# Kernel optimization log

Measured on AMD Instinct MI355X. Metric: run time of the kernel, lower is better.

The kernel has to match this reference:

```python
import jax, jax.numpy as jnp
import numpy as np

N, E, D, L, G = 10000, 320000, 256, 5, 128
RWSE, DEG_V = 16, 1001
BN_EPS = 1e-5


def setup_inputs() -> dict:
    key = jax.random.key(0)
    ks = jax.random.split(key, 12)
    s = 1.0 / np.sqrt(D)
    return {
        'feat_id': jax.random.randint(ks[0], (N,), 0, 100000, dtype=jnp.int64 if jax.config.jax_enable_x64 else jnp.int32),
        'edge_index': jax.random.randint(ks[1], (2, E), 0, N),
        'batch_idx': jnp.sort(jax.random.randint(ks[2], (N,), 0, G)),
        'rwse': jax.random.normal(ks[3], (N, RWSE), jnp.float32),
        'in_degrees': jax.random.randint(ks[4], (N,), 0, DEG_V),
        # value_projection: Linear(fixed_input_dim=D -> D); stored as [in, out]
        'w_val': jax.random.normal(ks[5], (D, D), jnp.float32) * s,
        'b_val': jnp.zeros((D,), jnp.float32),
        # rwse_projection: Linear(RWSE -> D)
        'w_rwse': jax.random.normal(ks[6], (RWSE, D), jnp.float32) * (1.0 / np.sqrt(RWSE)),
        'b_rwse': jnp.zeros((D,), jnp.float32),
        # degree_embedding table (clamped to [0, 1000])
        'deg_emb': jax.random.normal(ks[7], (DEG_V, D), jnp.float32) * 0.02,
        # per-layer GIN MLP: Linear-ReLU-Linear, stacked over L layers
        'mlp_w1': jax.random.normal(ks[8], (L, D, D), jnp.float32) * s,
        'mlp_b1': jnp.zeros((L, D), jnp.float32),
        'mlp_w2': jax.random.normal(ks[9], (L, D, D), jnp.float32) * s,
        'mlp_b2': jnp.zeros((L, D), jnp.float32),
        # BatchNorm1d (eval mode: running stats)
        'bn_gamma': jnp.ones((L, D), jnp.float32),
        'bn_beta': jnp.zeros((L, D), jnp.float32),
        'bn_mean': jnp.zeros((L, D), jnp.float32),
        'bn_var': jax.random.uniform(ks[10], (L, D), jnp.float32, 0.5, 1.5),
        # GIN eps per layer
        'eps_gin': jnp.zeros((L,), jnp.float32),
    }


def reference(feat_id, edge_index, batch_idx, rwse, in_degrees,
              w_val, b_val, w_rwse, b_rwse, deg_emb,
              mlp_w1, mlp_b1, mlp_w2, mlp_b2,
              bn_gamma, bn_beta, bn_mean, bn_var, eps_gin):
    # --- node feature embedding ---
    h_id = jnp.remainder(feat_id, D)
    h_one = jax.nn.one_hot(h_id, D, dtype=jnp.float32)            # [N, D]
    h = h_one @ w_val + b_val + rwse @ w_rwse + b_rwse            # value + rwse projections
    deg = jnp.clip(in_degrees, 0, 1000)
    h = h + deg_emb[deg]                                          # degree embedding

    src, dst = edge_index[0], edge_index[1]
    for l in range(L):
        # GIN message passing: sum neighbor features into dst (gather -> scatter-add)
        agg = jax.ops.segment_sum(h[src], dst, num_segments=N)    # [N, D]
        y = agg + (1.0 + eps_gin[l]) * h
        # MLP (Linear-ReLU-Linear)
        y = jax.nn.relu(y @ mlp_w1[l] + mlp_b1[l]) @ mlp_w2[l] + mlp_b2[l]
        # BatchNorm1d (eval: running stats) + ReLU
        y = (y - bn_mean[l]) * (bn_gamma[l] * jax.lax.rsqrt(bn_var[l] + BN_EPS)) + bn_beta[l]
        h = jax.nn.relu(y)

    # --- mean pooling per graph ---
    sums = jax.ops.segment_sum(h, batch_idx, num_segments=G)                     # [G, D]
    cnt = jax.ops.segment_sum(jnp.ones((N, 1), h.dtype), batch_idx, num_segments=G)
    graph_feature = sums / jnp.maximum(cnt, 1.0)
    return graph_feature, h
```

## Files before the change

### kernel.cpp

```cpp
#include <hip/hip_runtime.h>
#include <hip/hip_bf16.h>

#define N_NODES 10000
#define N_EDGES 320000
#define DIM     256
#define N_LAYERS 5
#define N_GRAPHS 128
#define RWSE_K  16

typedef __bf16 bf16_t;
typedef bf16_t bf16x8 __attribute__((ext_vector_type(8)));
typedef float  f32x4  __attribute__((ext_vector_type(4)));

__device__ inline ushort f2bf(float f) {
    union { float f; unsigned u; } v; v.f = f;
    unsigned r = v.u + 0x7fff + ((v.u >> 16) & 1);
    return (ushort)(r >> 16);
}
__device__ inline float bfbits2f(unsigned hi16) {
    union { unsigned u; float f; } v; v.u = hi16;
    return v.f;
}

__global__ __launch_bounds__(256)
void setup_kernel(const int* __restrict__ feat_id,
                  const float* __restrict__ rwse,
                  const int* __restrict__ in_deg,
                  const float* __restrict__ w_val,
                  const float* __restrict__ b_val,
                  const float* __restrict__ w_rwse,
                  const float* __restrict__ b_rwse,
                  const float* __restrict__ deg_emb,
                  float* __restrict__ h, ushort* __restrict__ hb,
                  const int* __restrict__ ei, int* __restrict__ cnt_arr,
                  const float* __restrict__ w1, const float* __restrict__ w2,
                  ushort* __restrict__ wt1, ushort* __restrict__ wt2,
                  const float* __restrict__ gamma, const float* __restrict__ beta,
                  const float* __restrict__ mean, const float* __restrict__ var,
                  const float* __restrict__ b2, float* __restrict__ scale,
                  float* __restrict__ shift) {
    __shared__ float r[RWSE_K];
    __shared__ float t[32][33];
    int b = blockIdx.x;
    int tid = threadIdx.x;
    if (b < N_NODES) {
        int i = b, d = tid;
        if (d < RWSE_K) r[d] = rwse[i * RWSE_K + d];
        __syncthreads();
        int hid = feat_id[i] & (DIM - 1);
        int dg = in_deg[i];
        dg = dg < 0 ? 0 : (dg > 1000 ? 1000 : dg);
        float v = w_val[hid * DIM + d] + b_val[d] + b_rwse[d] + deg_emb[dg * DIM + d];
#pragma unroll
        for (int k = 0; k < RWSE_K; ++k) v += r[k] * w_rwse[k * DIM + d];
        h[i * DIM + d] = v;
        hb[i * DIM + d] = f2bf(v);
    } else if (b < 11250) {
        int e = (b - N_NODES) * 256 + tid;
        if (e < N_EDGES) atomicAdd(&cnt_arr[ei[N_EDGES + e]], 1);
    } else if (b < 11890) {
        int w_id = b - 11250;
        int l = w_id >> 7;
        int rem = w_id & 127;
        int mat = rem >> 6;
        int tile = rem & 63;
        const float* W  = (mat ? w2  : w1)  + (size_t)l * DIM * DIM;
        ushort*      Wt = (mat ? wt2 : wt1) + (size_t)l * DIM * DIM;
        int k0 = (tile >> 3) * 32, n0 = (tile & 7) * 32;
        int tx = tid & 31, ty = tid >> 5;
#pragma unroll
        for (int j = 0; j < 4; ++j)
            t[ty + j * 8][tx] = W[(k0 + ty + j * 8) * DIM + n0 + tx];
        __syncthreads();
#pragma unroll
        for (int j = 0; j < 4; ++j)
            Wt[(n0 + ty + j * 8) * DIM + k0 + tx] = f2bf(t[tx][ty + j * 8]);
    } else {
        int l = b - 11890;
        int idx = l * DIM + tid;
        float s = gamma[idx] * rsqrtf(var[idx] + 1e-5f);
        scale[idx] = s;
        shift[idx] = beta[idx] + (b2[idx] - mean[idx]) * s;
    }
}

__global__ __launch_bounds__(1024)
void scan_kernel(const int* __restrict__ cnt_arr, int* __restrict__ cur, int n) {
    __shared__ int wsum[16];
    __shared__ int carry_sh;
    int tid = threadIdx.x, wave = tid >> 6, lane = tid & 63;
    if (tid == 0) carry_sh = 0;
    __syncthreads();
    for (int base = 0; base < n; base += 1024) {
        int idx = base + tid;
        int v = (idx < n) ? cnt_arr[idx] : 0;
        int s = v;
#pragma unroll
        for (int off = 1; off < 64; off <<= 1) {
            int t = __shfl_up(s, off, 64);
            if (lane >= off) s += t;
        }
        if (lane == 63) wsum[wave] = s;
        __syncthreads();
        if (wave == 0) {
            int ws = (lane < 16) ? wsum[lane] : 0;
#pragma unroll
            for (int off = 1; off < 16; off <<= 1) {
                int t = __shfl_up(ws, off, 64);
                if (lane >= off) ws += t;
            }
            if (lane < 16) wsum[lane] = ws;
        }
        __syncthreads();
        int excl = s - v + (wave ? wsum[wave - 1] : 0) + carry_sh;
        if (idx < n) cur[idx] = excl;
        __syncthreads();
        if (tid == 0) carry_sh += wsum[15];
        __syncthreads();
    }
}

__global__ __launch_bounds__(256)
void fill_kernel(const int* __restrict__ ei, int* __restrict__ cur,
                 int* __restrict__ cs) {
    int e = blockIdx.x * 256 + threadIdx.x;
    if (e < N_EDGES) {
        int d = ei[N_EDGES + e];
        int p = atomicAdd(&cur[d], 1);
        cs[p] = ei[e];
    }
}

__global__ __launch_bounds__(256)
void agg_kernel(const float* __restrict__ h, const ushort* __restrict__ hb,
                const int* __restrict__ cur, const int* __restrict__ cs,
                const float* __restrict__ eps_gin, int layer,
                ushort* __restrict__ y) {
    int wave = threadIdx.x >> 6;
    int lane = threadIdx.x & 63;
    int half = lane >> 5;
    int sl   = lane & 31;
    int i = blockIdx.x * 4 + wave;
    if (i >= N_NODES) return;
    const uint4* hb4 = (const uint4*)hb;
    float acc[8];
#pragma unroll
    for (int t = 0; t < 8; ++t) acc[t] = 0.f;

    int e0 = i ? cur[i - 1] : 0;
    int e1 = cur[i];
    for (int base = e0; base < e1; base += 64) {
        int rem = e1 - base;
        int cnt = rem < 64 ? rem : 64;
        int idx = (base + lane < e1) ? cs[base + lane] : 0;
        int j = 0;
        for (; j + 8 <= cnt; j += 8) {
            int s0 = __shfl(idx, j + half, 64);
            int s1 = __shfl(idx, j + 2 + half, 64);
            int s2 = __shfl(idx, j + 4 + half, 64);
            int s3 = __shfl(idx, j + 6 + half, 64);
            uint4 v0 = hb4[(size_t)s0 * 32 + sl];
            uint4 v1 = hb4[(size_t)s1 * 32 + sl];
            uint4 v2 = hb4[(size_t)s2 * 32 + sl];
            uint4 v3 = hb4[(size_t)s3 * 32 + sl];
            acc[0] += bfbits2f(v0.x << 16); acc[1] += bfbits2f(v0.x & 0xffff0000u);
            acc[2] += bfbits2f(v0.y << 16); acc[3] += bfbits2f(v0.y & 0xffff0000u);
            acc[4] += bfbits2f(v0.z << 16); acc[5] += bfbits2f(v0.z & 0xffff0000u);
            acc[6] += bfbits2f(v0.w << 16); acc[7] += bfbits2f(v0.w & 0xffff0000u);
            acc[0] += bfbits2f(v1.x << 16); acc[1] += bfbits2f(v1.x & 0xffff0000u);
            acc[2] += bfbits2f(v1.y << 16); acc[3] += bfbits2f(v1.y & 0xffff0000u);
            acc[4] += bfbits2f(v1.z << 16); acc[5] += bfbits2f(v1.z & 0xffff0000u);
            acc[6] += bfbits2f(v1.w << 16); acc[7] += bfbits2f(v1.w & 0xffff0000u);
            acc[0] += bfbits2f(v2.x << 16); acc[1] += bfbits2f(v2.x & 0xffff0000u);
            acc[2] += bfbits2f(v2.y << 16); acc[3] += bfbits2f(v2.y & 0xffff0000u);
            acc[4] += bfbits2f(v2.z << 16); acc[5] += bfbits2f(v2.z & 0xffff0000u);
            acc[6] += bfbits2f(v2.w << 16); acc[7] += bfbits2f(v2.w & 0xffff0000u);
            acc[0] += bfbits2f(v3.x << 16); acc[1] += bfbits2f(v3.x & 0xffff0000u);
            acc[2] += bfbits2f(v3.y << 16); acc[3] += bfbits2f(v3.y & 0xffff0000u);
            acc[4] += bfbits2f(v3.z << 16); acc[5] += bfbits2f(v3.z & 0xffff0000u);
            acc[6] += bfbits2f(v3.w << 16); acc[7] += bfbits2f(v3.w & 0xffff0000u);
        }
        for (; j + 2 <= cnt; j += 2) {
            int s = __shfl(idx, j + half, 64);
            uint4 v = hb4[(size_t)s * 32 + sl];
            acc[0] += bfbits2f(v.x << 16); acc[1] += bfbits2f(v.x & 0xffff0000u);
            acc[2] += bfbits2f(v.y << 16); acc[3] += bfbits2f(v.y & 0xffff0000u);
            acc[4] += bfbits2f(v.z << 16); acc[5] += bfbits2f(v.z & 0xffff0000u);
            acc[6] += bfbits2f(v.w << 16); acc[7] += bfbits2f(v.w & 0xffff0000u);
        }
        if (j < cnt) {
            int s = __shfl(idx, j, 64);
            if (half == 0) {
                uint4 v = hb4[(size_t)s * 32 + sl];
                acc[0] += bfbits2f(v.x << 16); acc[1] += bfbits2f(v.x & 0xffff0000u);
                acc[2] += bfbits2f(v.y << 16); acc[3] += bfbits2f(v.y & 0xffff0000u);
                acc[4] += bfbits2f(v.z << 16); acc[5] += bfbits2f(v.z & 0xffff0000u);
                acc[6] += bfbits2f(v.w << 16); acc[7] += bfbits2f(v.w & 0xffff0000u);
            }
        }
    }
#pragma unroll
    for (int t = 0; t < 8; ++t) acc[t] += __shfl_xor(acc[t], 32, 64);
    if (half == 0) {
        float sc = 1.0f + eps_gin[layer];
        const float4* h4 = (const float4*)h;
        float4 a0 = h4[(size_t)i * 64 + sl * 2];
        float4 a1 = h4[(size_t)i * 64 + sl * 2 + 1];
        acc[0] += a0.x * sc; acc[1] += a0.y * sc;
        acc[2] += a0.z * sc; acc[3] += a0.w * sc;
        acc[4] += a1.x * sc; acc[5] += a1.y * sc;
        acc[6] += a1.z * sc; acc[7] += a1.w * sc;
        uint4 o;
        o.x = (uint)f2bf(acc[0]) | ((uint)f2bf(acc[1]) << 16);
        o.y = (uint)f2bf(acc[2]) | ((uint)f2bf(acc[3]) << 16);
        o.z = (uint)f2bf(acc[4]) | ((uint)f2bf(acc[5]) << 16);
        o.w = (uint)f2bf(acc[6]) | ((uint)f2bf(acc[7]) << 16);
        ((uint4*)y)[(size_t)i * 32 + sl] = o;
    }
}

#define GBM 32

__global__ __launch_bounds__(256)
void gemm12_kernel(const ushort* __restrict__ A, const ushort* __restrict__ Wt1,
                   const float* __restrict__ b1, const ushort* __restrict__ Wt2,
                   const float* __restrict__ bnsc, const float* __restrict__ bnsh,
                   float* __restrict__ H, ushort* __restrict__ Hb, int nrows) {
    __shared__ __align__(16) ushort As[GBM][40];
    __shared__ __align__(16) ushort Bs[DIM][40];
    __shared__ __align__(16) ushort Ts[GBM][DIM + 8];
    int tx = threadIdx.x;
    int row0 = blockIdx.x * GBM;
    int wave = tx >> 6, lane = tx & 63, quad = lane >> 4, l16 = lane & 15;
    int wr = (wave >> 1) * 16;
    int wc = (wave & 1) * 128;
    int srow = tx >> 2;
    int skol = (tx & 3) * 8;

    f32x4 acc[8];
#pragma unroll
    for (int t = 0; t < 8; ++t) acc[t] = (f32x4){0.f, 0.f, 0.f, 0.f};

    for (int k0 = 0; k0 < DIM; k0 += 32) {
        if (tx < 128) {
            int arow = row0 + srow;
            uint4 av = make_uint4(0u, 0u, 0u, 0u);
            if (arow < nrows) av = *(const uint4*)&A[(size_t)arow * DIM + k0 + skol];
            *(uint4*)&As[srow][skol] = av;
        }
#pragma unroll
        for (int j = 0; j < 4; ++j) {
            int r = srow + 64 * j;
            *(uint4*)&Bs[r][skol] = *(const uint4*)&Wt1[(size_t)r * DIM + k0 + skol];
        }
        __syncthreads();
        bf16x8 af = *(const bf16x8*)&As[wr + l16][quad * 8];
#pragma unroll
        for (int tj = 0; tj < 8; ++tj) {
            bf16x8 bf = *(const bf16x8*)&Bs[wc + tj * 16 + l16][quad * 8];
            acc[tj] = __builtin_amdgcn_mfma_f32_16x16x32_bf16(af, bf, acc[tj], 0, 0, 0);
        }
        __syncthreads();
    }
#pragma unroll
    for (int tj = 0; tj < 8; ++tj) {
        int col = wc + tj * 16 + l16;
        float bias = b1[col];
#pragma unroll
        for (int r = 0; r < 4; ++r) {
            int rl = wr + quad * 4 + r;
            Ts[rl][col] = f2bf(fmaxf(acc[tj][r] + bias, 0.f));
        }
    }
    __syncthreads();

#pragma unroll
    for (int t = 0; t < 8; ++t) acc[t] = (f32x4){0.f, 0.f, 0.f, 0.f};
    for (int k0 = 0; k0 < DIM; k0 += 32) {
#pragma unroll
        for (int j = 0; j < 4; ++j) {
            int r = srow + 64 * j;
            *(uint4*)&Bs[r][skol] = *(const uint4*)&Wt2[(size_t)r * DIM + k0 + skol];
        }
        __syncthreads();
        bf16x8 af = *(const bf16x8*)&Ts[wr + l16][k0 + quad * 8];
#pragma unroll
        for (int tj = 0; tj < 8; ++tj) {
            bf16x8 bf = *(const bf16x8*)&Bs[wc + tj * 16 + l16][quad * 8];
            acc[tj] = __builtin_amdgcn_mfma_f32_16x16x32_bf16(af, bf, acc[tj], 0, 0, 0);
        }
        __syncthreads();
    }
#pragma unroll
    for (int tj = 0; tj < 8; ++tj) {
        int col = wc + tj * 16 + l16;
        float s = bnsc[col], sh = bnsh[col];
#pragma unroll
        for (int r = 0; r < 4; ++r) {
            int row = row0 + wr + quad * 4 + r;
            if (row < nrows) {
                float v = fmaxf(acc[tj][r] * s + sh, 0.f);
                H[(size_t)row * DIM + col] = v;
                Hb[(size_t)row * DIM + col] = f2bf(v);
            }
        }
    }
}

__global__ __launch_bounds__(256)
void pool_kernel(const float* __restrict__ hfin, const int* __restrict__ batch,
                 float* __restrict__ out) {
    int g = blockIdx.x;
    int d = threadIdx.x;
    int l = 0, r = N_NODES;
    while (l < r) { int m = (l + r) >> 1; if (batch[m] < g) l = m + 1; else r = m; }
    int lo = l;
    r = N_NODES;
    while (l < r) { int m = (l + r) >> 1; if (batch[m] < g + 1) l = m + 1; else r = m; }
    int hi = l;
    float a0 = 0.f, a1 = 0.f, a2 = 0.f, a3 = 0.f;
    int i = lo;
    for (; i + 4 <= hi; i += 4) {
        a0 += hfin[(size_t)i * DIM + d];
        a1 += hfin[(size_t)(i + 1) * DIM + d];
        a2 += hfin[(size_t)(i + 2) * DIM + d];
        a3 += hfin[(size_t)(i + 3) * DIM + d];
    }
    for (; i < hi; ++i) a0 += hfin[(size_t)i * DIM + d];
    float c = (float)(hi - lo);
    if (c < 1.f) c = 1.f;
    out[g * DIM + d] = ((a0 + a1) + (a2 + a3)) / c;
}

extern "C" void kernel_launch(void* const* d_in, const int* in_sizes, int n_in,
                              void* d_out, int out_size, void* d_ws, size_t ws_size,
                              hipStream_t stream) {
    const int*   feat_id  = (const int*)d_in[0];
    const int*   ei       = (const int*)d_in[1];
    const int*   batch    = (const int*)d_in[2];
    const float* rwse     = (const float*)d_in[3];
    const int*   in_deg   = (const int*)d_in[4];
    const float* w_val    = (const float*)d_in[5];
    const float* b_val    = (const float*)d_in[6];
    const float* w_rwse   = (const float*)d_in[7];
    const float* b_rwse   = (const float*)d_in[8];
    const float* deg_emb  = (const float*)d_in[9];
    const float* mlp_w1   = (const float*)d_in[10];
    const float* mlp_b1   = (const float*)d_in[11];
    const float* mlp_w2   = (const float*)d_in[12];
    const float* mlp_b2   = (const float*)d_in[13];
    const float* bn_gamma = (const float*)d_in[14];
    const float* bn_beta  = (const float*)d_in[15];
    const float* bn_mean  = (const float*)d_in[16];
    const float* bn_var   = (const float*)d_in[17];
    const float* eps_gin  = (const float*)d_in[18];

    float* out = (float*)d_out;
    float* out_h = out + N_GRAPHS * DIM;

    char* w = (char*)d_ws;
    float*  h   = (float*)w;
    ushort* hb  = (ushort*)(h + (size_t)N_NODES * DIM);
    ushort* y   = hb + (size_t)N_NODES * DIM;
    ushort* wt1 = y + (size_t)N_NODES * DIM;
    ushort* wt2 = wt1 + (size_t)N_LAYERS * DIM * DIM;
    int* cnt_arr = (int*)(wt2 + (size_t)N_LAYERS * DIM * DIM);
    int* cur     = cnt_arr + N_NODES;
    int* cs      = cur + N_NODES;
    float* bnsc  = (float*)(cs + N_EDGES);
    float* bnsh  = bnsc + N_LAYERS * DIM;

    hipMemsetAsync(cnt_arr, 0, N_NODES * sizeof(int), stream);

    setup_kernel<<<11895, 256, 0, stream>>>(
        feat_id, rwse, in_deg, w_val, b_val, w_rwse, b_rwse, deg_emb, h, hb,
        ei, cnt_arr, mlp_w1, mlp_w2, wt1, wt2,
        bn_gamma, bn_beta, bn_mean, bn_var, mlp_b2, bnsc, bnsh);
    scan_kernel<<<1, 1024, 0, stream>>>(cnt_arr, cur, N_NODES);
    fill_kernel<<<(N_EDGES + 255) / 256, 256, 0, stream>>>(ei, cur, cs);

    int ggrid = (N_NODES + GBM - 1) / GBM;
    for (int l = 0; l < N_LAYERS; ++l) {
        agg_kernel<<<(N_NODES + 3) / 4, 256, 0, stream>>>(h, hb, cur, cs, eps_gin, l, y);
        float* Hdst = (l == N_LAYERS - 1) ? out_h : h;
        gemm12_kernel<<<ggrid, 256, 0, stream>>>(y, wt1 + (size_t)l * DIM * DIM,
                                                 mlp_b1 + l * DIM,
                                                 wt2 + (size_t)l * DIM * DIM,
                                                 bnsc + l * DIM, bnsh + l * DIM,
                                                 Hdst, hb, N_NODES);
    }

    pool_kernel<<<N_GRAPHS, 256, 0, stream>>>(out_h, batch, out);
}
```

Measured before the change: 362.7 us.

## Replace LDS-staged MLP GEMM with single-wave register-tiled kernel; scalarize agg index loads

The fused two-GEMM MLP kernel is rewritten so that one 64-thread wave owns a 32-row tile. It reads A and weight fragments straight from global memory instead of staging them through shared memory, and keeps 32 accumulators in registers, which removes the block-wide __syncthreads barriers. The aggregation kernel makes the edge range wave-uniform and loads neighbor indices directly instead of shuffling them, and the bf16 copy of h is no longer written on the last layer. The trade-offs are heavy register pressure, low occupancy from 64-thread blocks, and weight reads that now depend on L1/L2 hits rather than LDS reuse.

Result: slower. 610.0 us (+68.2%).

```diff
diff --git a/kernel.cpp b/kernel.cpp
--- a/kernel.cpp
+++ b/kernel.cpp
@@ -131,6 +131,12 @@
     }
 }
 
+#define ACCV(v)                                                        \
+    acc[0] += bfbits2f((v).x << 16); acc[1] += bfbits2f((v).x & 0xffff0000u); \
+    acc[2] += bfbits2f((v).y << 16); acc[3] += bfbits2f((v).y & 0xffff0000u); \
+    acc[4] += bfbits2f((v).z << 16); acc[5] += bfbits2f((v).z & 0xffff0000u); \
+    acc[6] += bfbits2f((v).w << 16); acc[7] += bfbits2f((v).w & 0xffff0000u);
+
 __global__ __launch_bounds__(256)
 void agg_kernel(const float* __restrict__ h, const ushort* __restrict__ hb,
                 const int* __restrict__ cur, const int* __restrict__ cs,
@@ -149,54 +155,34 @@
 
     int e0 = i ? cur[i - 1] : 0;
     int e1 = cur[i];
-    for (int base = e0; base < e1; base += 64) {
-        int rem = e1 - base;
-        int cnt = rem < 64 ? rem : 64;
-        int idx = (base + lane < e1) ? cs[base + lane] : 0;
-        int j = 0;
-        for (; j + 8 <= cnt; j += 8) {
-            int s0 = __shfl(idx, j + half, 64);
-            int s1 = __shfl(idx, j + 2 + half, 64);
-            int s2 = __shfl(idx, j + 4 + half, 64);
-            int s3 = __shfl(idx, j + 6 + half, 64);
-            uint4 v0 = hb4[(size_t)s0 * 32 + sl];
-            uint4 v1 = hb4[(size_t)s1 * 32 + sl];
-            uint4 v2 = hb4[(size_t)s2 * 32 + sl];
-            uint4 v3 = hb4[(size_t)s3 * 32 + sl];
-            acc[0] += bfbits2f(v0.x << 16); acc[1] += bfbits2f(v0.x & 0xffff0000u);
-            acc[2] += bfbits2f(v0.y << 16); acc[3] += bfbits2f(v0.y & 0xffff0000u);
-            acc[4] += bfbits2f(v0.z << 16); acc[5] += bfbits2f(v0.z & 0xffff0000u);
-            acc[6] += bfbits2f(v0.w << 16); acc[7] += bfbits2f(v0.w & 0xffff0000u);
-            acc[0] += bfbits2f(v1.x << 16); acc[1] += bfbits2f(v1.x & 0xffff0000u);
-            acc[2] += bfbits2f(v1.y << 16); acc[3] += bfbits2f(v1.y & 0xffff0000u);
-            acc[4] += bfbits2f(v1.z << 16); acc[5] += bfbits2f(v1.z & 0xffff0000u);
-            acc[6] += bfbits2f(v1.w << 16); acc[7] += bfbits2f(v1.w & 0xffff0000u);
-            acc[0] += bfbits2f(v2.x << 16); acc[1] += bfbits2f(v2.x & 0xffff0000u);
-            acc[2] += bfbits2f(v2.y << 16); acc[3] += bfbits2f(v2.y & 0xffff0000u);
-            acc[4] += bfbits2f(v2.z << 16); acc[5] += bfbits2f(v2.z & 0xffff0000u);
-            acc[6] += bfbits2f(v2.w << 16); acc[7] += bfbits2f(v2.w & 0xffff0000u);
-            acc[0] += bfbits2f(v3.x << 16); acc[1] += bfbits2f(v3.x & 0xffff0000u);
-            acc[2] += bfbits2f(v3.y << 16); acc[3] += bfbits2f(v3.y & 0xffff0000u);
-            acc[4] += bfbits2f(v3.z << 16); acc[5] += bfbits2f(v3.z & 0xffff0000u);
-            acc[6] += bfbits2f(v3.w << 16); acc[7] += bfbits2f(v3.w & 0xffff0000u);
-        }
-        for (; j + 2 <= cnt; j += 2) {
-            int s = __shfl(idx, j + half, 64);
-            uint4 v = hb4[(size_t)s * 32 + sl];
-            acc[0] += bfbits2f(v.x << 16); acc[1] += bfbits2f(v.x & 0xffff0000u);
-            acc[2] += bfbits2f(v.y << 16); acc[3] += bfbits2f(v.y & 0xffff0000u);
-            acc[4] += bfbits2f(v.z << 16); acc[5] += bfbits2f(v.z & 0xffff0000u);
-            acc[6] += bfbits2f(v.w << 16); acc[7] += bfbits2f(v.w & 0xffff0000u);
-        }
-        if (j < cnt) {
-            int s = __shfl(idx, j, 64);
-            if (half == 0) {
-                uint4 v = hb4[(size_t)s * 32 + sl];
-                acc[0] += bfbits2f(v.x << 16); acc[1] += bfbits2f(v.x & 0xffff0000u);
-                acc[2] += bfbits2f(v.y << 16); acc[3] += bfbits2f(v.y & 0xffff0000u);
-                acc[4] += bfbits2f(v.z << 16); acc[5] += bfbits2f(v.z & 0xffff0000u);
-                acc[6] += bfbits2f(v.w << 16); acc[7] += bfbits2f(v.w & 0xffff0000u);
-            }
+    e0 = __builtin_amdgcn_readfirstlane(e0);
+    e1 = __builtin_amdgcn_readfirstlane(e1);
+
+    int e = e0;
+    for (; e + 8 <= e1; e += 8) {
+        int n0 = cs[e + 0], n1 = cs[e + 1], n2 = cs[e + 2], n3 = cs[e + 3];
+        int n4 = cs[e + 4], n5 = cs[e + 5], n6 = cs[e + 6], n7 = cs[e + 7];
+        int s0 = half ? n1 : n0;
+        int s1 = half ? n3 : n2;
+        int s2 = half ? n5 : n4;
+        int s3 = half ? n7 : n6;
+        uint4 v0 = hb4[(size_t)s0 * 32 + sl];
+        uint4 v1 = hb4[(size_t)s1 * 32 + sl];
+        uint4 v2 = hb4[(size_t)s2 * 32 + sl];
+        uint4 v3 = hb4[(size_t)s3 * 32 + sl];
+        ACCV(v0); ACCV(v1); ACCV(v2); ACCV(v3);
+    }
+    for (; e + 2 <= e1; e += 2) {
+        int n0 = cs[e], n1 = cs[e + 1];
+        int s = half ? n1 : n0;
+        uint4 v = hb4[(size_t)s * 32 + sl];
+        ACCV(v);
+    }
+    if (e < e1) {
+        int n0 = cs[e];
+        if (!half) {
+            uint4 v = hb4[(size_t)n0 * 32 + sl];
+            ACCV(v);
         }
     }
 #pragma unroll
@@ -219,91 +205,81 @@
     }
 }
 
-#define GBM 32
-
-__global__ __launch_bounds__(256)
-void gemm12_kernel(const ushort* __restrict__ A, const ushort* __restrict__ Wt1,
-                   const float* __restrict__ b1, const ushort* __restrict__ Wt2,
-                   const float* __restrict__ bnsc, const float* __restrict__ bnsh,
-                   float* __restrict__ H, ushort* __restrict__ Hb, int nrows) {
-    __shared__ __align__(16) ushort As[GBM][40];
-    __shared__ __align__(16) ushort Bs[DIM][40];
-    __shared__ __align__(16) ushort Ts[GBM][DIM + 8];
-    int tx = threadIdx.x;
-    int row0 = blockIdx.x * GBM;
-    int wave = tx >> 6, lane = tx & 63, quad = lane >> 4, l16 = lane & 15;
-    int wr = (wave >> 1) * 16;
-    int wc = (wave & 1) * 128;
-    int srow = tx >> 2;
-    int skol = (tx & 3) * 8;
-
-    f32x4 acc[8];
-#pragma unroll
-    for (int t = 0; t < 8; ++t) acc[t] = (f32x4){0.f, 0.f, 0.f, 0.f};
+#define MROWS 32
+#define MTILES ((N_NODES + MROWS - 1) / MROWS)
+
+__global__ __launch_bounds__(64)
+void mlp_kernel(const ushort* __restrict__ A, const ushort* __restrict__ Wt1,
+                const float* __restrict__ b1, const ushort* __restrict__ Wt2,
+                const float* __restrict__ bnsc, const float* __restrict__ bnsh,
+                float* __restrict__ H, ushort* __restrict__ Hb, int nrows) {
+    __shared__ __align__(16) ushort t_lds[MROWS][DIM + 8];
+    int lane = threadIdx.x;
+    int quad = lane >> 4, l16 = lane & 15;
+    int row0 = blockIdx.x * MROWS;
+    int r0 = row0 + l16;
+    int r1 = row0 + 16 + l16;
+
+    f32x4 acc[2][16];
+#pragma unroll
+    for (int mg = 0; mg < 2; ++mg)
+#pragma unroll
+        for (int tj = 0; tj < 16; ++tj) acc[mg][tj] = (f32x4){0.f, 0.f, 0.f, 0.f};
+
+    const bf16x8 zf = (bf16x8){0, 0, 0, 0, 0, 0, 0, 0};
 
     for (int k0 = 0; k0 < DIM; k0 += 32) {
-        if (tx < 128) {
-            int arow = row0 + srow;
-            uint4 av = make_uint4(0u, 0u, 0u, 0u);
-            if (arow < nrows) av = *(const uint4*)&A[(size_t)arow * DIM + k0 + skol];
-            *(uint4*)&As[srow][skol] = av;
-        }
-#pragma unroll
-        for (int j = 0; j < 4; ++j) {
-            int r = srow + 64 * j;
-            *(uint4*)&Bs[r][skol] = *(const uint4*)&Wt1[(size_t)r * DIM + k0 + skol];
-        }
-        __syncthreads();
-        bf16x8 af = *(const bf16x8*)&As[wr + l16][quad * 8];
-#pragma unroll
-        for (int tj = 0; tj < 8; ++tj) {
-            bf16x8 bf = *(const bf16x8*)&Bs[wc + tj * 16 + l16][quad * 8];
-            acc[tj] = __builtin_amdgcn_mfma_f32_16x16x32_bf16(af, bf, acc[tj], 0, 0, 0);
-        }
-        __syncthreads();
-    }
-#pragma unroll
-    for (int tj = 0; tj < 8; ++tj) {
-        int col = wc + tj * 16 + l16;
+        int ko = k0 + quad * 8;
+        bf16x8 a0 = (r0 < nrows) ? *(const bf16x8*)&A[(size_t)r0 * DIM + ko] : zf;
+        bf16x8 a1 = (r1 < nrows) ? *(const bf16x8*)&A[(size_t)r1 * DIM + ko] : zf;
+#pragma unroll
+        for (int tj = 0; tj < 16; ++tj) {
+            bf16x8 bfr = *(const bf16x8*)&Wt1[(size_t)(tj * 16 + l16) * DIM + ko];
+            acc[0][tj] = __builtin_amdgcn_mfma_f32_16x16x32_bf16(a0, bfr, acc[0][tj], 0, 0, 0);
+            acc[1][tj] = __builtin_amdgcn_mfma_f32_16x16x32_bf16(a1, bfr, acc[1][tj], 0, 0, 0);
+        }
+    }
+#pragma unroll
+    for (int tj = 0; tj < 16; ++tj) {
+        int col = tj * 16 + l16;
         float bias = b1[col];
 #pragma unroll
-        for (int r = 0; r < 4; ++r) {
-            int rl = wr + quad * 4 + r;
-            Ts[rl][col] = f2bf(fmaxf(acc[tj][r] + bias, 0.f));
-        }
-    }
-    __syncthreads();
-
-#pragma unroll
-    for (int t = 0; t < 8; ++t) acc[t] = (f32x4){0.f, 0.f, 0.f, 0.f};
+        for (int mg = 0; mg < 2; ++mg)
+#pragma unroll
+            for (int r = 0; r < 4; ++r)
+                t_lds[mg * 16 + quad * 4 + r][col] = f2bf(fmaxf(acc[mg][tj][r] + bias, 0.f));
+    }
+
+#pragma unroll
+    for (int mg = 0; mg < 2; ++mg)
+#pragma unroll
+        for (int tj = 0; tj < 16; ++tj) acc[mg][tj] = (f32x4){0.f, 0.f, 0.f, 0.f};
     for (int k0 = 0; k0 < DIM; k0 += 32) {
-#pragma unroll
-        for (int j = 0; j < 4; ++j) {
-            int r = srow + 64 * j;
-            *(uint4*)&Bs[r][skol] = *(const uint4*)&Wt2[(size_t)r * DIM + k0 + skol];
-        }
-        __syncthreads();
-        bf16x8 af = *(const bf16x8*)&Ts[wr + l16][k0 + quad * 8];
-#pragma unroll
-        for (int tj = 0; tj < 8; ++tj) {
-            bf16x8 bf = *(const bf16x8*)&Bs[wc + tj * 16 + l16][quad * 8];
-            acc[tj] = __builtin_amdgcn_mfma_f32_16x16x32_bf16(af, bf, acc[tj], 0, 0, 0);
-        }
-        __syncthreads();
-    }
-#pragma unroll
-    for (int tj = 0; tj < 8; ++tj) {
-        int col = wc + tj * 16 + l16;
+        int ko = k0 + quad * 8;
+        bf16x8 a0 = *(const bf16x8*)&t_lds[l16][ko];
+        bf16x8 a1 = *(const bf16x8*)&t_lds[16 + l16][ko];
+#pragma unroll
+        for (int tj = 0; tj < 16; ++tj) {
+            bf16x8 bfr = *(const bf16x8*)&Wt2[(size_t)(tj * 16 + l16) * DIM + ko];
+            acc[0][tj] = __builtin_amdgcn_mfma_f32_16x16x32_bf16(a0, bfr, acc[0][tj], 0, 0, 0);
+            acc[1][tj] = __builtin_amdgcn_mfma_f32_16x16x32_bf16(a1, bfr, acc[1][tj], 0, 0, 0);
+        }
+    }
+#pragma unroll
+    for (int tj = 0; tj < 16; ++tj) {
+        int col = tj * 16 + l16;
         float s = bnsc[col], sh = bnsh[col];
 #pragma unroll
-        for (int r = 0; r < 4; ++r) {
-            int row = row0 + wr + quad * 4 + r;
-            if (row < nrows) {
-                float v = fmaxf(acc[tj][r] * s + sh, 0.f);
-                H[(size_t)row * DIM + col] = v;
-                Hb[(size_t)row * DIM + col] = f2bf(v);
+        for (int mg = 0; mg < 2; ++mg)
+#pragma unroll
+            for (int r = 0; r < 4; ++r) {
+                int row = row0 + mg * 16 + quad * 4 + r;
+                if (row < nrows) {
+                    float v = fmaxf(acc[mg][tj][r] * s + sh, 0.f);
+                    H[(size_t)row * DIM + col] = v;
+                    if (Hb) Hb[(size_t)row * DIM + col] = f2bf(v);
+                }
             }
-        }
     }
 }
 
@@ -379,15 +355,15 @@
     scan_kernel<<<1, 1024, 0, stream>>>(cnt_arr, cur, N_NODES);
     fill_kernel<<<(N_EDGES + 255) / 256, 256, 0, stream>>>(ei, cur, cs);
 
-    int ggrid = (N_NODES + GBM - 1) / GBM;
     for (int l = 0; l < N_LAYERS; ++l) {
         agg_kernel<<<(N_NODES + 3) / 4, 256, 0, stream>>>(h, hb, cur, cs, eps_gin, l, y);
         float* Hdst = (l == N_LAYERS - 1) ? out_h : h;
-        gemm12_kernel<<<ggrid, 256, 0, stream>>>(y, wt1 + (size_t)l * DIM * DIM,
-                                                 mlp_b1 + l * DIM,
-                                                 wt2 + (size_t)l * DIM * DIM,
-                                                 bnsc + l * DIM, bnsh + l * DIM,
-                                                 Hdst, hb, N_NODES);
+        ushort* Hbdst = (l == N_LAYERS - 1) ? nullptr : hb;
+        mlp_kernel<<<MTILES, 64, 0, stream>>>(y, wt1 + (size_t)l * DIM * DIM,
+                                              mlp_b1 + l * DIM,
+                                              wt2 + (size_t)l * DIM * DIM,
+                                              bnsc + l * DIM, bnsh + l * DIM,
+                                              Hdst, Hbdst, N_NODES);
     }
 
     pool_kernel<<<N_GRAPHS, 256, 0, stream>>>(out_h, batch, out);
```

## Split bf16 node features into column halves and aggregate each half separately

Applied to the files above, without the earlier changes.

Node features are stored as two separate bf16 arrays, one per 128-column half, and the gather-aggregate kernel runs twice per layer, once per half. Each gathered table is half the size, so it is more likely to stay in cache during the random neighbor gather. The fp32 copy of h is dropped: the self term now reads the bf16 copy, and the GEMM writes fp32 output only on the last layer. The cost is an extra kernel launch per layer, repeated CSR index reads, and slightly lower precision in the self term.

After: 382.1 us. +5.4%, slower.

```diff
diff --git a/kernel.cpp b/kernel.cpp
--- a/kernel.cpp
+++ b/kernel.cpp
@@ -4,6 +4,7 @@
 #define N_NODES 10000
 #define N_EDGES 320000
 #define DIM     256
+#define HDIM    128
 #define N_LAYERS 5
 #define N_GRAPHS 128
 #define RWSE_K  16
@@ -31,7 +32,7 @@
                   const float* __restrict__ w_rwse,
                   const float* __restrict__ b_rwse,
                   const float* __restrict__ deg_emb,
-                  float* __restrict__ h, ushort* __restrict__ hb,
+                  ushort* __restrict__ hb_lo, ushort* __restrict__ hb_hi,
                   const int* __restrict__ ei, int* __restrict__ cnt_arr,
                   const float* __restrict__ w1, const float* __restrict__ w2,
                   ushort* __restrict__ wt1, ushort* __restrict__ wt2,
@@ -53,8 +54,8 @@
         float v = w_val[hid * DIM + d] + b_val[d] + b_rwse[d] + deg_emb[dg * DIM + d];
 #pragma unroll
         for (int k = 0; k < RWSE_K; ++k) v += r[k] * w_rwse[k * DIM + d];
-        h[i * DIM + d] = v;
-        hb[i * DIM + d] = f2bf(v);
+        int hh = d >> 7, dl = d & (HDIM - 1);
+        (hh ? hb_hi : hb_lo)[i * HDIM + dl] = f2bf(v);
     } else if (b < 11250) {
         int e = (b - N_NODES) * 256 + tid;
         if (e < N_EDGES) atomicAdd(&cnt_arr[ei[N_EDGES + e]], 1);
@@ -131,18 +132,24 @@
     }
 }
 
-__global__ __launch_bounds__(256)
-void agg_kernel(const float* __restrict__ h, const ushort* __restrict__ hb,
+#define ACCV(v)                                                        \
+    acc[0] += bfbits2f((v).x << 16); acc[1] += bfbits2f((v).x & 0xffff0000u); \
+    acc[2] += bfbits2f((v).y << 16); acc[3] += bfbits2f((v).y & 0xffff0000u); \
+    acc[4] += bfbits2f((v).z << 16); acc[5] += bfbits2f((v).z & 0xffff0000u); \
+    acc[6] += bfbits2f((v).w << 16); acc[7] += bfbits2f((v).w & 0xffff0000u);
+
+__global__ __launch_bounds__(256)
+void agg_kernel(const ushort* __restrict__ hbH,
                 const int* __restrict__ cur, const int* __restrict__ cs,
-                const float* __restrict__ eps_gin, int layer,
+                const float* __restrict__ eps_gin, int layer, int hh,
                 ushort* __restrict__ y) {
     int wave = threadIdx.x >> 6;
     int lane = threadIdx.x & 63;
-    int half = lane >> 5;
-    int sl   = lane & 31;
+    int quarter = lane >> 4;
+    int sl = lane & 15;
     int i = blockIdx.x * 4 + wave;
     if (i >= N_NODES) return;
-    const uint4* hb4 = (const uint4*)hb;
+    const uint4* hb4 = (const uint4*)hbH;
     float acc[8];
 #pragma unroll
     for (int t = 0; t < 8; ++t) acc[t] = 0.f;
@@ -155,67 +162,42 @@
         int idx = (base + lane < e1) ? cs[base + lane] : 0;
         int j = 0;
         for (; j + 8 <= cnt; j += 8) {
-            int s0 = __shfl(idx, j + half, 64);
-            int s1 = __shfl(idx, j + 2 + half, 64);
-            int s2 = __shfl(idx, j + 4 + half, 64);
-            int s3 = __shfl(idx, j + 6 + half, 64);
-            uint4 v0 = hb4[(size_t)s0 * 32 + sl];
-            uint4 v1 = hb4[(size_t)s1 * 32 + sl];
-            uint4 v2 = hb4[(size_t)s2 * 32 + sl];
-            uint4 v3 = hb4[(size_t)s3 * 32 + sl];
-            acc[0] += bfbits2f(v0.x << 16); acc[1] += bfbits2f(v0.x & 0xffff0000u);
-            acc[2] += bfbits2f(v0.y << 16); acc[3] += bfbits2f(v0.y & 0xffff0000u);
-            acc[4] += bfbits2f(v0.z << 16); acc[5] += bfbits2f(v0.z & 0xffff0000u);
-            acc[6] += bfbits2f(v0.w << 16); acc[7] += bfbits2f(v0.w & 0xffff0000u);
-            acc[0] += bfbits2f(v1.x << 16); acc[1] += bfbits2f(v1.x & 0xffff0000u);
-            acc[2] += bfbits2f(v1.y << 16); acc[3] += bfbits2f(v1.y & 0xffff0000u);
-            acc[4] += bfbits2f(v1.z << 16); acc[5] += bfbits2f(v1.z & 0xffff0000u);
-            acc[6] += bfbits2f(v1.w << 16); acc[7] += bfbits2f(v1.w & 0xffff0000u);
-            acc[0] += bfbits2f(v2.x << 16); acc[1] += bfbits2f(v2.x & 0xffff0000u);
-            acc[2] += bfbits2f(v2.y << 16); acc[3] += bfbits2f(v2.y & 0xffff0000u);
-            acc[4] += bfbits2f(v2.z << 16); acc[5] += bfbits2f(v2.z & 0xffff0000u);
-            acc[6] += bfbits2f(v2.w << 16); acc[7] += bfbits2f(v2.w & 0xffff0000u);
-            acc[0] += bfbits2f(v3.x << 16); acc[1] += bfbits2f(v3.x & 0xffff0000u);
-            acc[2] += bfbits2f(v3.y << 16); acc[3] += bfbits2f(v3.y & 0xffff0000u);
-            acc[4] += bfbits2f(v3.z << 16); acc[5] += bfbits2f(v3.z & 0xffff0000u);
-            acc[6] += bfbits2f(v3.w << 16); acc[7] += bfbits2f(v3.w & 0xffff0000u);
-        }
-        for (; j + 2 <= cnt; j += 2) {
-            int s = __shfl(idx, j + half, 64);
-            uint4 v = hb4[(size_t)s * 32 + sl];
-            acc[0] += bfbits2f(v.x << 16); acc[1] += bfbits2f(v.x & 0xffff0000u);
-            acc[2] += bfbits2f(v.y << 16); acc[3] += bfbits2f(v.y & 0xffff0000u);
-            acc[4] += bfbits2f(v.z << 16); acc[5] += bfbits2f(v.z & 0xffff0000u);
-            acc[6] += bfbits2f(v.w << 16); acc[7] += bfbits2f(v.w & 0xffff0000u);
-        }
-        if (j < cnt) {
+            int s0 = __shfl(idx, j + quarter, 64);
+            int s1 = __shfl(idx, j + 4 + quarter, 64);
+            uint4 v0 = hb4[(size_t)s0 * 16 + sl];
+            uint4 v1 = hb4[(size_t)s1 * 16 + sl];
+            ACCV(v0); ACCV(v1);
+        }
+        for (; j + 4 <= cnt; j += 4) {
+            int s = __shfl(idx, j + quarter, 64);
+            uint4 v = hb4[(size_t)s * 16 + sl];
+            ACCV(v);
+        }
+        for (; j < cnt; ++j) {
             int s = __shfl(idx, j, 64);
-            if (half == 0) {
-                uint4 v = hb4[(size_t)s * 32 + sl];
-                acc[0] += bfbits2f(v.x << 16); acc[1] += bfbits2f(v.x & 0xffff0000u);
-                acc[2] += bfbits2f(v.y << 16); acc[3] += bfbits2f(v.y & 0xffff0000u);
-                acc[4] += bfbits2f(v.z << 16); acc[5] += bfbits2f(v.z & 0xffff0000u);
-                acc[6] += bfbits2f(v.w << 16); acc[7] += bfbits2f(v.w & 0xffff0000u);
+            if (quarter == 0) {
+                uint4 v = hb4[(size_t)s * 16 + sl];
+                ACCV(v);
             }
         }
     }
 #pragma unroll
+    for (int t = 0; t < 8; ++t) acc[t] += __shfl_xor(acc[t], 16, 64);
+#pragma unroll
     for (int t = 0; t < 8; ++t) acc[t] += __shfl_xor(acc[t], 32, 64);
-    if (half == 0) {
+    if (quarter == 0) {
         float sc = 1.0f + eps_gin[layer];
-        const float4* h4 = (const float4*)h;
-        float4 a0 = h4[(size_t)i * 64 + sl * 2];
-        float4 a1 = h4[(size_t)i * 64 + sl * 2 + 1];
-        acc[0] += a0.x * sc; acc[1] += a0.y * sc;
-        acc[2] += a0.z * sc; acc[3] += a0.w * sc;
-        acc[4] += a1.x * sc; acc[5] += a1.y * sc;
-        acc[6] += a1.z * sc; acc[7] += a1.w * sc;
+        uint4 sv = hb4[(size_t)i * 16 + sl];
+        acc[0] += bfbits2f(sv.x << 16) * sc; acc[1] += bfbits2f(sv.x & 0xffff0000u) * sc;
+        acc[2] += bfbits2f(sv.y << 16) * sc; acc[3] += bfbits2f(sv.y & 0xffff0000u) * sc;
+        acc[4] += bfbits2f(sv.z << 16) * sc; acc[5] += bfbits2f(sv.z & 0xffff0000u) * sc;
+        acc[6] += bfbits2f(sv.w << 16) * sc; acc[7] += bfbits2f(sv.w & 0xffff0000u) * sc;
         uint4 o;
         o.x = (uint)f2bf(acc[0]) | ((uint)f2bf(acc[1]) << 16);
         o.y = (uint)f2bf(acc[2]) | ((uint)f2bf(acc[3]) << 16);
         o.z = (uint)f2bf(acc[4]) | ((uint)f2bf(acc[5]) << 16);
         o.w = (uint)f2bf(acc[6]) | ((uint)f2bf(acc[7]) << 16);
-        ((uint4*)y)[(size_t)i * 32 + sl] = o;
+        ((uint4*)y)[(size_t)i * 32 + hh * 16 + sl] = o;
     }
 }
 
@@ -225,7 +207,8 @@
 void gemm12_kernel(const ushort* __restrict__ A, const ushort* __restrict__ Wt1,
                    const float* __restrict__ b1, const ushort* __restrict__ Wt2,
                    const float* __restrict__ bnsc, const float* __restrict__ bnsh,
-                   float* __restrict__ H, ushort* __restrict__ Hb, int nrows) {
+                   float* __restrict__ outF, ushort* __restrict__ hbl,
+                   ushort* __restrict__ hbh, int nrows) {
     __shared__ __align__(16) ushort As[GBM][40];
     __shared__ __align__(16) ushort Bs[DIM][40];
     __shared__ __align__(16) ushort Ts[GBM][DIM + 8];
@@ -300,8 +283,11 @@
             int row = row0 + wr + quad * 4 + r;
             if (row < nrows) {
                 float v = fmaxf(acc[tj][r] * s + sh, 0.f);
-                H[(size_t)row * DIM + col] = v;
-                Hb[(size_t)row * DIM + col] = f2bf(v);
+                if (outF) outF[(size_t)row * DIM + col] = v;
+                if (hbl) {
+                    if (col < HDIM) hbl[(size_t)row * HDIM + col] = f2bf(v);
+                    else            hbh[(size_t)row * HDIM + col - HDIM] = f2bf(v);
+                }
             }
         }
     }
@@ -359,35 +345,37 @@
     float* out_h = out + N_GRAPHS * DIM;
 
     char* w = (char*)d_ws;
-    float*  h   = (float*)w;
-    ushort* hb  = (ushort*)(h + (size_t)N_NODES * DIM);
-    ushort* y   = hb + (size_t)N_NODES * DIM;
-    ushort* wt1 = y + (size_t)N_NODES * DIM;
-    ushort* wt2 = wt1 + (size_t)N_LAYERS * DIM * DIM;
-    int* cnt_arr = (int*)(wt2 + (size_t)N_LAYERS * DIM * DIM);
-    int* cur     = cnt_arr + N_NODES;
-    int* cs      = cur + N_NODES;
-    float* bnsc  = (float*)(cs + N_EDGES);
-    float* bnsh  = bnsc + N_LAYERS * DIM;
+    ushort* hb_lo = (ushort*)w;
+    ushort* hb_hi = hb_lo + (size_t)N_NODES * HDIM;
+    ushort* y     = hb_hi + (size_t)N_NODES * HDIM;
+    ushort* wt1   = y + (size_t)N_NODES * DIM;
+    ushort* wt2   = wt1 + (size_t)N_LAYERS * DIM * DIM;
+    int* cnt_arr  = (int*)(wt2 + (size_t)N_LAYERS * DIM * DIM);
+    int* cur      = cnt_arr + N_NODES;
+    int* cs       = cur + N_NODES;
+    float* bnsc   = (float*)(cs + N_EDGES);
+    float* bnsh   = bnsc + N_LAYERS * DIM;
 
     hipMemsetAsync(cnt_arr, 0, N_NODES * sizeof(int), stream);
 
     setup_kernel<<<11895, 256, 0, stream>>>(
-        feat_id, rwse, in_deg, w_val, b_val, w_rwse, b_rwse, deg_emb, h, hb,
-        ei, cnt_arr, mlp_w1, mlp_w2, wt1, wt2,
+        feat_id, rwse, in_deg, w_val, b_val, w_rwse, b_rwse, deg_emb,
+        hb_lo, hb_hi, ei, cnt_arr, mlp_w1, mlp_w2, wt1, wt2,
         bn_gamma, bn_beta, bn_mean, bn_var, mlp_b2, bnsc, bnsh);
     scan_kernel<<<1, 1024, 0, stream>>>(cnt_arr, cur, N_NODES);
     fill_kernel<<<(N_EDGES + 255) / 256, 256, 0, stream>>>(ei, cur, cs);
 
+    int agrid = (N_NODES + 3) / 4;
     int ggrid = (N_NODES + GBM - 1) / GBM;
     for (int l = 0; l < N_LAYERS; ++l) {
-        agg_kernel<<<(N_NODES + 3) / 4, 256, 0, stream>>>(h, hb, cur, cs, eps_gin, l, y);
-        float* Hdst = (l == N_LAYERS - 1) ? out_h : h;
-        gemm12_kernel<<<ggrid, 256, 0, stream>>>(y, wt1 + (size_t)l * DIM * DIM,
-                                                 mlp_b1 + l * DIM,
-                                                 wt2 + (size_t)l * DIM * DIM,
-                                                 bnsc + l * DIM, bnsh + l * DIM,
-                                                 Hdst, hb, N_NODES);
+        agg_kernel<<<agrid, 256, 0, stream>>>(hb_lo, cur, cs, eps_gin, l, 0, y);
+        agg_kernel<<<agrid, 256, 0, stream>>>(hb_hi, cur, cs, eps_gin, l, 1, y);
+        bool last = (l == N_LAYERS - 1);
+        gemm12_kernel<<<ggrid, 256, 0, stream>>>(
+            y, wt1 + (size_t)l * DIM * DIM, mlp_b1 + l * DIM,
+            wt2 + (size_t)l * DIM * DIM, bnsc + l * DIM, bnsh + l * DIM,
+            last ? out_h : nullptr,
+            last ? nullptr : hb_lo, last ? nullptr : hb_hi, N_NODES);
     }
 
     pool_kernel<<<N_GRAPHS, 256, 0, stream>>>(out_h, batch, out);
```

## Drop fp32 hidden-state copy and shrink fused MLP row tile to 16

Applied to the files above, without the earlier changes.

The fp32 copy of the node features is removed. The self term in aggregation now reads the bf16 copy, and intermediate layers write only bf16, with fp32 written only for the final layer output. This cuts global write and read traffic per layer. The fused two-GEMM MLP kernel also moves from 32-row to 16-row blocks with each wave covering 64 columns, doubling the grid for better CU occupancy but reloading the weights from memory twice as often. The self term loses precision because it is now read as bf16.

New measurement: 342.7 us. 1.06x faster.

```diff
diff --git a/kernel.cpp b/kernel.cpp
--- a/kernel.cpp
+++ b/kernel.cpp
@@ -7,6 +7,7 @@
 #define N_LAYERS 5
 #define N_GRAPHS 128
 #define RWSE_K  16
+#define GBM 16
 
 typedef __bf16 bf16_t;
 typedef bf16_t bf16x8 __attribute__((ext_vector_type(8)));
@@ -31,7 +32,7 @@
                   const float* __restrict__ w_rwse,
                   const float* __restrict__ b_rwse,
                   const float* __restrict__ deg_emb,
-                  float* __restrict__ h, ushort* __restrict__ hb,
+                  ushort* __restrict__ hb,
                   const int* __restrict__ ei, int* __restrict__ cnt_arr,
                   const float* __restrict__ w1, const float* __restrict__ w2,
                   ushort* __restrict__ wt1, ushort* __restrict__ wt2,
@@ -53,7 +54,6 @@
         float v = w_val[hid * DIM + d] + b_val[d] + b_rwse[d] + deg_emb[dg * DIM + d];
 #pragma unroll
         for (int k = 0; k < RWSE_K; ++k) v += r[k] * w_rwse[k * DIM + d];
-        h[i * DIM + d] = v;
         hb[i * DIM + d] = f2bf(v);
     } else if (b < 11250) {
         int e = (b - N_NODES) * 256 + tid;
@@ -131,8 +131,14 @@
     }
 }
 
-__global__ __launch_bounds__(256)
-void agg_kernel(const float* __restrict__ h, const ushort* __restrict__ hb,
+#define ACCV(v)                                                        \
+    acc[0] += bfbits2f((v).x << 16); acc[1] += bfbits2f((v).x & 0xffff0000u); \
+    acc[2] += bfbits2f((v).y << 16); acc[3] += bfbits2f((v).y & 0xffff0000u); \
+    acc[4] += bfbits2f((v).z << 16); acc[5] += bfbits2f((v).z & 0xffff0000u); \
+    acc[6] += bfbits2f((v).w << 16); acc[7] += bfbits2f((v).w & 0xffff0000u);
+
+__global__ __launch_bounds__(256)
+void agg_kernel(const ushort* __restrict__ hb,
                 const int* __restrict__ cur, const int* __restrict__ cs,
                 const float* __restrict__ eps_gin, int layer,
                 ushort* __restrict__ y) {
@@ -163,39 +169,18 @@
             uint4 v1 = hb4[(size_t)s1 * 32 + sl];
             uint4 v2 = hb4[(size_t)s2 * 32 + sl];
             uint4 v3 = hb4[(size_t)s3 * 32 + sl];
-            acc[0] += bfbits2f(v0.x << 16); acc[1] += bfbits2f(v0.x & 0xffff0000u);
-            acc[2] += bfbits2f(v0.y << 16); acc[3] += bfbits2f(v0.y & 0xffff0000u);
-            acc[4] += bfbits2f(v0.z << 16); acc[5] += bfbits2f(v0.z & 0xffff0000u);
-            acc[6] += bfbits2f(v0.w << 16); acc[7] += bfbits2f(v0.w & 0xffff0000u);
-            acc[0] += bfbits2f(v1.x << 16); acc[1] += bfbits2f(v1.x & 0xffff0000u);
-            acc[2] += bfbits2f(v1.y << 16); acc[3] += bfbits2f(v1.y & 0xffff0000u);
-            acc[4] += bfbits2f(v1.z << 16); acc[5] += bfbits2f(v1.z & 0xffff0000u);
-            acc[6] += bfbits2f(v1.w << 16); acc[7] += bfbits2f(v1.w & 0xffff0000u);
-            acc[0] += bfbits2f(v2.x << 16); acc[1] += bfbits2f(v2.x & 0xffff0000u);
-            acc[2] += bfbits2f(v2.y << 16); acc[3] += bfbits2f(v2.y & 0xffff0000u);
-            acc[4] += bfbits2f(v2.z << 16); acc[5] += bfbits2f(v2.z & 0xffff0000u);
-            acc[6] += bfbits2f(v2.w << 16); acc[7] += bfbits2f(v2.w & 0xffff0000u);
-            acc[0] += bfbits2f(v3.x << 16); acc[1] += bfbits2f(v3.x & 0xffff0000u);
-            acc[2] += bfbits2f(v3.y << 16); acc[3] += bfbits2f(v3.y & 0xffff0000u);
-            acc[4] += bfbits2f(v3.z << 16); acc[5] += bfbits2f(v3.z & 0xffff0000u);
-            acc[6] += bfbits2f(v3.w << 16); acc[7] += bfbits2f(v3.w & 0xffff0000u);
+            ACCV(v0); ACCV(v1); ACCV(v2); ACCV(v3);
         }
         for (; j + 2 <= cnt; j += 2) {
             int s = __shfl(idx, j + half, 64);
             uint4 v = hb4[(size_t)s * 32 + sl];
-            acc[0] += bfbits2f(v.x << 16); acc[1] += bfbits2f(v.x & 0xffff0000u);
-            acc[2] += bfbits2f(v.y << 16); acc[3] += bfbits2f(v.y & 0xffff0000u);
-            acc[4] += bfbits2f(v.z << 16); acc[5] += bfbits2f(v.z & 0xffff0000u);
-            acc[6] += bfbits2f(v.w << 16); acc[7] += bfbits2f(v.w & 0xffff0000u);
+            ACCV(v);
         }
         if (j < cnt) {
             int s = __shfl(idx, j, 64);
             if (half == 0) {
                 uint4 v = hb4[(size_t)s * 32 + sl];
-                acc[0] += bfbits2f(v.x << 16); acc[1] += bfbits2f(v.x & 0xffff0000u);
-                acc[2] += bfbits2f(v.y << 16); acc[3] += bfbits2f(v.y & 0xffff0000u);
-                acc[4] += bfbits2f(v.z << 16); acc[5] += bfbits2f(v.z & 0xffff0000u);
-                acc[6] += bfbits2f(v.w << 16); acc[7] += bfbits2f(v.w & 0xffff0000u);
+                ACCV(v);
             }
         }
     }
@@ -203,13 +188,11 @@
     for (int t = 0; t < 8; ++t) acc[t] += __shfl_xor(acc[t], 32, 64);
     if (half == 0) {
         float sc = 1.0f + eps_gin[layer];
-        const float4* h4 = (const float4*)h;
-        float4 a0 = h4[(size_t)i * 64 + sl * 2];
-        float4 a1 = h4[(size_t)i * 64 + sl * 2 + 1];
-        acc[0] += a0.x * sc; acc[1] += a0.y * sc;
-        acc[2] += a0.z * sc; acc[3] += a0.w * sc;
-        acc[4] += a1.x * sc; acc[5] += a1.y * sc;
-        acc[6] += a1.z * sc; acc[7] += a1.w * sc;
+        uint4 sv = hb4[(size_t)i * 32 + sl];
+        acc[0] += bfbits2f(sv.x << 16) * sc; acc[1] += bfbits2f(sv.x & 0xffff0000u) * sc;
+        acc[2] += bfbits2f(sv.y << 16) * sc; acc[3] += bfbits2f(sv.y & 0xffff0000u) * sc;
+        acc[4] += bfbits2f(sv.z << 16) * sc; acc[5] += bfbits2f(sv.z & 0xffff0000u) * sc;
+        acc[6] += bfbits2f(sv.w << 16) * sc; acc[7] += bfbits2f(sv.w & 0xffff0000u) * sc;
         uint4 o;
         o.x = (uint)f2bf(acc[0]) | ((uint)f2bf(acc[1]) << 16);
         o.y = (uint)f2bf(acc[2]) | ((uint)f2bf(acc[3]) << 16);
@@ -219,30 +202,27 @@
     }
 }
 
-#define GBM 32
-
 __global__ __launch_bounds__(256)
 void gemm12_kernel(const ushort* __restrict__ A, const ushort* __restrict__ Wt1,
                    const float* __restrict__ b1, const ushort* __restrict__ Wt2,
                    const float* __restrict__ bnsc, const float* __restrict__ bnsh,
-                   float* __restrict__ H, ushort* __restrict__ Hb, int nrows) {
+                   float* __restrict__ outF, ushort* __restrict__ outB, int nrows) {
     __shared__ __align__(16) ushort As[GBM][40];
     __shared__ __align__(16) ushort Bs[DIM][40];
     __shared__ __align__(16) ushort Ts[GBM][DIM + 8];
     int tx = threadIdx.x;
     int row0 = blockIdx.x * GBM;
     int wave = tx >> 6, lane = tx & 63, quad = lane >> 4, l16 = lane & 15;
-    int wr = (wave >> 1) * 16;
-    int wc = (wave & 1) * 128;
+    int wc = wave * 64;
     int srow = tx >> 2;
     int skol = (tx & 3) * 8;
 
-    f32x4 acc[8];
-#pragma unroll
-    for (int t = 0; t < 8; ++t) acc[t] = (f32x4){0.f, 0.f, 0.f, 0.f};
+    f32x4 acc[4];
+#pragma unroll
+    for (int t = 0; t < 4; ++t) acc[t] = (f32x4){0.f, 0.f, 0.f, 0.f};
 
     for (int k0 = 0; k0 < DIM; k0 += 32) {
-        if (tx < 128) {
+        if (tx < 64) {
             int arow = row0 + srow;
             uint4 av = make_uint4(0u, 0u, 0u, 0u);
             if (arow < nrows) av = *(const uint4*)&A[(size_t)arow * DIM + k0 + skol];
@@ -254,28 +234,26 @@
             *(uint4*)&Bs[r][skol] = *(const uint4*)&Wt1[(size_t)r * DIM + k0 + skol];
         }
         __syncthreads();
-        bf16x8 af = *(const bf16x8*)&As[wr + l16][quad * 8];
-#pragma unroll
-        for (int tj = 0; tj < 8; ++tj) {
+        bf16x8 af = *(const bf16x8*)&As[l16][quad * 8];
+#pragma unroll
+        for (int tj = 0; tj < 4; ++tj) {
             bf16x8 bf = *(const bf16x8*)&Bs[wc + tj * 16 + l16][quad * 8];
             acc[tj] = __builtin_amdgcn_mfma_f32_16x16x32_bf16(af, bf, acc[tj], 0, 0, 0);
         }
         __syncthreads();
     }
 #pragma unroll
-    for (int tj = 0; tj < 8; ++tj) {
+    for (int tj = 0; tj < 4; ++tj) {
         int col = wc + tj * 16 + l16;
         float bias = b1[col];
 #pragma unroll
-        for (int r = 0; r < 4; ++r) {
-            int rl = wr + quad * 4 + r;
-            Ts[rl][col] = f2bf(fmaxf(acc[tj][r] + bias, 0.f));
-        }
+        for (int r = 0; r < 4; ++r)
+            Ts[quad * 4 + r][col] = f2bf(fmaxf(acc[tj][r] + bias, 0.f));
     }
     __syncthreads();
 
 #pragma unroll
-    for (int t = 0; t < 8; ++t) acc[t] = (f32x4){0.f, 0.f, 0.f, 0.f};
+    for (int t = 0; t < 4; ++t) acc[t] = (f32x4){0.f, 0.f, 0.f, 0.f};
     for (int k0 = 0; k0 < DIM; k0 += 32) {
 #pragma unroll
         for (int j = 0; j < 4; ++j) {
@@ -283,25 +261,25 @@
             *(uint4*)&Bs[r][skol] = *(const uint4*)&Wt2[(size_t)r * DIM + k0 + skol];
         }
         __syncthreads();
-        bf16x8 af = *(const bf16x8*)&Ts[wr + l16][k0 + quad * 8];
-#pragma unroll
-        for (int tj = 0; tj < 8; ++tj) {
+        bf16x8 af = *(const bf16x8*)&Ts[l16][k0 + quad * 8];
+#pragma unroll
+        for (int tj = 0; tj < 4; ++tj) {
             bf16x8 bf = *(const bf16x8*)&Bs[wc + tj * 16 + l16][quad * 8];
             acc[tj] = __builtin_amdgcn_mfma_f32_16x16x32_bf16(af, bf, acc[tj], 0, 0, 0);
         }
         __syncthreads();
     }
 #pragma unroll
-    for (int tj = 0; tj < 8; ++tj) {
+    for (int tj = 0; tj < 4; ++tj) {
         int col = wc + tj * 16 + l16;
         float s = bnsc[col], sh = bnsh[col];
 #pragma unroll
         for (int r = 0; r < 4; ++r) {
-            int row = row0 + wr + quad * 4 + r;
+            int row = row0 + quad * 4 + r;
             if (row < nrows) {
                 float v = fmaxf(acc[tj][r] * s + sh, 0.f);
-                H[(size_t)row * DIM + col] = v;
-                Hb[(size_t)row * DIM + col] = f2bf(v);
+                if (outF) outF[(size_t)row * DIM + col] = v;
+                if (outB) outB[(size_t)row * DIM + col] = f2bf(v);
             }
         }
     }
@@ -359,11 +337,10 @@
     float* out_h = out + N_GRAPHS * DIM;
 
     char* w = (char*)d_ws;
-    float*  h   = (float*)w;
-    ushort* hb  = (ushort*)(h + (size_t)N_NODES * DIM);
-    ushort* y   = hb + (size_t)N_NODES * DIM;
-    ushort* wt1 = y + (size_t)N_NODES * DIM;
-    ushort* wt2 = wt1 + (size_t)N_LAYERS * DIM * DIM;
+    ushort* hb   = (ushort*)w;
+    ushort* y    = hb + (size_t)N_NODES * DIM;
+    ushort* wt1  = y + (size_t)N_NODES * DIM;
+    ushort* wt2  = wt1 + (size_t)N_LAYERS * DIM * DIM;
     int* cnt_arr = (int*)(wt2 + (size_t)N_LAYERS * DIM * DIM);
     int* cur     = cnt_arr + N_NODES;
     int* cs      = cur + N_NODES;
@@ -373,21 +350,21 @@
     hipMemsetAsync(cnt_arr, 0, N_NODES * sizeof(int), stream);
 
     setup_kernel<<<11895, 256, 0, stream>>>(
-        feat_id, rwse, in_deg, w_val, b_val, w_rwse, b_rwse, deg_emb, h, hb,
-        ei, cnt_arr, mlp_w1, mlp_w2, wt1, wt2,
+        feat_id, rwse, in_deg, w_val, b_val, w_rwse, b_rwse, deg_emb,
+        hb, ei, cnt_arr, mlp_w1, mlp_w2, wt1, wt2,
         bn_gamma, bn_beta, bn_mean, bn_var, mlp_b2, bnsc, bnsh);
     scan_kernel<<<1, 1024, 0, stream>>>(cnt_arr, cur, N_NODES);
     fill_kernel<<<(N_EDGES + 255) / 256, 256, 0, stream>>>(ei, cur, cs);
 
+    int agrid = (N_NODES + 3) / 4;
     int ggrid = (N_NODES + GBM - 1) / GBM;
     for (int l = 0; l < N_LAYERS; ++l) {
-        agg_kernel<<<(N_NODES + 3) / 4, 256, 0, stream>>>(h, hb, cur, cs, eps_gin, l, y);
-        float* Hdst = (l == N_LAYERS - 1) ? out_h : h;
-        gemm12_kernel<<<ggrid, 256, 0, stream>>>(y, wt1 + (size_t)l * DIM * DIM,
-                                                 mlp_b1 + l * DIM,
-                                                 wt2 + (size_t)l * DIM * DIM,
-                                                 bnsc + l * DIM, bnsh + l * DIM,
-                                                 Hdst, hb, N_NODES);
+        agg_kernel<<<agrid, 256, 0, stream>>>(hb, cur, cs, eps_gin, l, y);
+        bool last = (l == N_LAYERS - 1);
+        gemm12_kernel<<<ggrid, 256, 0, stream>>>(
+            y, wt1 + (size_t)l * DIM * DIM, mlp_b1 + l * DIM,
+            wt2 + (size_t)l * DIM * DIM, bnsc + l * DIM, bnsh + l * DIM,
+            last ? out_h : nullptr, last ? nullptr : hb, N_NODES);
     }
 
     pool_kernel<<<N_GRAPHS, 256, 0, stream>>>(out_h, batch, out);
```
